# Kernel optimization log

Measured on AMD Instinct MI355X. Metric: run time of the kernel, lower is better.

## Reference

```python
import jax, jax.numpy as jnp
import numpy as np

B = 4096          # batch of vectors
D = 768           # embedding_size
P = 96            # partition (number of sub-quantizers)
C = 256           # centroids per partition
SD = D // P       # sub-vector dim = 8


def setup_inputs() -> dict:
    key = jax.random.key(0)
    k1, k2 = jax.random.split(key)
    vecs = jax.random.normal(k1, (B, D), dtype=jnp.float32)
    # nn.Parameter(torch.empty(P, C, SD).uniform_(-0.1, 0.1))
    codebook = jax.random.uniform(k2, (P, C, SD), dtype=jnp.float32,
                                  minval=-0.1, maxval=0.1)
    return {"vecs": vecs, "codebook": codebook}


def _quantize(vecs, codebook):
    # vecs: [B, D] -> [B, P, SD]
    v = vecs.reshape(vecs.shape[0], P, SD)
    # proba = -sum((v - c)^2) expanded to avoid the [B,P,C,SD] intermediate:
    # ||v||^2 - 2 v.c + ||c||^2  per (b, p, c)
    v_sq = jnp.sum(v * v, axis=-1, keepdims=True)            # [B, P, 1]
    c_sq = jnp.sum(codebook * codebook, axis=-1)             # [P, C]
    vc = jnp.einsum('bpd,pcd->bpc', v, codebook)             # [B, P, C]
    proba = -(v_sq - 2.0 * vc + c_sq[None])                  # [B, P, C]
    assign = jax.nn.softmax(proba, axis=-1)                  # [B, P, C]
    # straight-through estimator: hard one-hot fwd, soft grad
    index = jnp.argmax(assign, axis=-1)                      # [B, P]
    assign_hard = jax.nn.one_hot(index, C, dtype=assign.dtype)
    assign_ste = jax.lax.stop_gradient(assign_hard - assign) + assign
    # reconstruction: [B,P,C] @ [P,C,SD] -> [B,P,SD] -> [B,D]
    q = jnp.einsum('bpc,pcd->bpd', assign_ste, codebook)
    return q.reshape(vecs.shape[0], -1)


def reference(vecs, codebook):
    return _quantize(vecs, codebook)
```

## Files before the change

kernel.cpp:

```cpp
#include <hip/hip_runtime.h>
#include <cmath>

constexpr int B  = 4096;
constexpr int D  = 768;
constexpr int P  = 96;
constexpr int C  = 256;
constexpr int SD = 8;

constexpr int TPB  = 64;
constexpr int ROWS = 4;

__device__ __forceinline__ float tree8(float q0, float q1, float q2, float q3,
                                       float q4, float q5, float q6, float q7)
{
#pragma clang fp contract(off)
    return ((q0 + q1) + (q2 + q3)) + ((q4 + q5) + (q6 + q7));
}

__device__ __forceinline__ float proba_np(const float* __restrict__ cbf,
                                          const float* __restrict__ csq,
                                          int c, float4 va, float4 vb, float vsq)
{
#pragma clang fp contract(off)
    float4 ca = ((const float4*)cbf)[2 * c];
    float4 cb = ((const float4*)cbf)[2 * c + 1];
    float p0 = va.x * ca.x, p1 = va.y * ca.y, p2 = va.z * ca.z, p3 = va.w * ca.w;
    float p4 = vb.x * cb.x, p5 = vb.y * cb.y, p6 = vb.z * cb.z, p7 = vb.w * cb.w;
    float l0 = p0 + p4, l1 = p1 + p5, l2 = p2 + p6, l3 = p3 + p7;
    float vc = (l0 + l2) + (l1 + l3);
    float tt = vsq - 2.0f * vc;
    float u  = tt + csq[c];
    return -u;
}

__device__ __attribute__((noinline))
int exact_search(const float* __restrict__ cbf, const float* __restrict__ csq,
                 float4 va, float4 vb, float vsq)
{
#pragma clang fp contract(off)
    float best = -3.402823466e38f, second = -3.402823466e38f;
    int bi = 0;
    for (int c = 0; c < C; ++c) {
        float pr = proba_np(cbf, csq, c, va, vb, vsq);
        if (pr > best)        { second = best; best = pr; bi = c; }
        else if (pr > second) { second = pr; }
    }
    int idx = bi;

    if (best - second <= 1.0e-6f) {
        float m = best;
        float r0[8] = {0,0,0,0,0,0,0,0};
        float r1[8] = {0,0,0,0,0,0,0,0};
        for (int cg = 0; cg < 16; ++cg) {
            #pragma unroll
            for (int j = 0; j < 8; ++j) {
                float pr = proba_np(cbf, csq, cg * 8 + j, va, vb, vsq);
                r0[j] += expf(pr - m);
            }
        }
        for (int cg = 16; cg < 32; ++cg) {
            #pragma unroll
            for (int j = 0; j < 8; ++j) {
                float pr = proba_np(cbf, csq, cg * 8 + j, va, vb, vsq);
                r1[j] += expf(pr - m);
            }
        }
        float sum = tree8(r0[0],r0[1],r0[2],r0[3],r0[4],r0[5],r0[6],r0[7])
                  + tree8(r1[0],r1[1],r1[2],r1[3],r1[4],r1[5],r1[6],r1[7]);
        float abest = -1.0f;
        int   ai    = 0;
        for (int c = 0; c < C; ++c) {
            float pr = proba_np(cbf, csq, c, va, vb, vsq);
            float e  = expf(pr - m);
            float a  = e / sum;
            if (a > abest) { abest = a; ai = c; }
        }
        idx = ai;
    }
    return idx;
}

__global__ __launch_bounds__(TPB, 8)
void pq_fast_kernel(const float* __restrict__ vecs,
                    const float* __restrict__ codebook,
                    float* __restrict__ out)
{
    __shared__ float cbf [C * SD];
    __shared__ float csqn[C];
    __shared__ float csqh[C];

    const int p = blockIdx.x;
    const int t = threadIdx.x;
    const int base = blockIdx.y * (TPB * ROWS);

    const float4* src = (const float4*)(codebook + (size_t)p * C * SD);
    #pragma unroll
    for (int i = 0; i < 8; ++i)
        ((float4*)cbf)[t + 64 * i] = src[t + 64 * i];
    __syncthreads();

    #pragma unroll
    for (int k = 0; k < 4; ++k) {
        int c = t + 64 * k;
        const float* cc = cbf + c * SD;
        float q0 = cc[0]*cc[0], q1 = cc[1]*cc[1], q2 = cc[2]*cc[2], q3 = cc[3]*cc[3];
        float q4 = cc[4]*cc[4], q5 = cc[5]*cc[5], q6 = cc[6]*cc[6], q7 = cc[7]*cc[7];
        float s = tree8(q0,q1,q2,q3,q4,q5,q6,q7);
        csqn[c] = s;
        csqh[c] = -0.5f * s;
    }
    __syncthreads();

    float4 va[ROWS], vb[ROWS];
    #pragma unroll
    for (int r = 0; r < ROWS; ++r) {
        const float* vptr = vecs + (size_t)(base + 64 * r + t) * D + (size_t)p * SD;
        va[r] = ((const float4*)vptr)[0];
        vb[r] = ((const float4*)vptr)[1];
    }

    float vsq[ROWS];
    #pragma unroll
    for (int r = 0; r < ROWS; ++r) {
        float q0 = va[r].x*va[r].x, q1 = va[r].y*va[r].y,
              q2 = va[r].z*va[r].z, q3 = va[r].w*va[r].w;
        float q4 = vb[r].x*vb[r].x, q5 = vb[r].y*vb[r].y,
              q6 = vb[r].z*vb[r].z, q7 = vb[r].w*vb[r].w;
        vsq[r] = tree8(q0,q1,q2,q3,q4,q5,q6,q7);
    }

    float best[ROWS], second[ROWS];
    int   bi[ROWS];
    #pragma unroll
    for (int r = 0; r < ROWS; ++r) {
        best[r] = -3.402823466e38f; second[r] = -3.402823466e38f; bi[r] = 0;
    }

    #pragma unroll 2
    for (int c = 0; c < C; ++c) {
        float4 ca = ((const float4*)cbf)[2 * c];
        float4 cb = ((const float4*)cbf)[2 * c + 1];
        float  ch = csqh[c];
        #pragma unroll
        for (int r = 0; r < ROWS; ++r) {
            float s = fmaf(va[r].x, ca.x, ch);
            s = fmaf(va[r].y, ca.y, s);
            s = fmaf(va[r].z, ca.z, s);
            s = fmaf(va[r].w, ca.w, s);
            s = fmaf(vb[r].x, cb.x, s);
            s = fmaf(vb[r].y, cb.y, s);
            s = fmaf(vb[r].z, cb.z, s);
            s = fmaf(vb[r].w, cb.w, s);
            bool gt = s > best[r];
            second[r] = fmaxf(second[r], fminf(s, best[r]));
            bi[r]     = gt ? c : bi[r];
            best[r]   = fmaxf(s, best[r]);
        }
    }

    #pragma unroll
    for (int r = 0; r < ROWS; ++r) {
        int idx = bi[r];
        if (best[r] - second[r] <= 2.0e-5f)
            idx = exact_search(cbf, csqn, va[r], vb[r], vsq[r]);
        float4 o0 = ((const float4*)cbf)[2 * idx];
        float4 o1 = ((const float4*)cbf)[2 * idx + 1];
        float4* op = (float4*)(out + (size_t)(base + 64 * r + t) * D + (size_t)p * SD);
        op[0] = o0;
        op[1] = o1;
    }
}

extern "C" void kernel_launch(void* const* d_in, const int* in_sizes, int n_in,
                              void* d_out, int out_size, void* d_ws, size_t ws_size,
                              hipStream_t stream)
{
    const float* vecs     = (const float*)d_in[0];
    const float* codebook = (const float*)d_in[1];
    float*       out      = (float*)d_out;

    dim3 grid(P, B / (TPB * ROWS));
    dim3 block(TPB);
    pq_fast_kernel<<<grid, block, 0, stream>>>(vecs, codebook, out);
}
```

Measured before the change: 193.9 us.

## Split centroid search across four waves with shared-memory argmax merge

Each block now runs four waves. Every wave scans a quarter of the 256 centroids for the same 256 rows, then the partial best/second/index values are merged through shared memory and the final winner is written out. The codebook shared-memory load is amortized over four times as many scanning threads per block, and each thread's serial loop is shortened, giving more parallel work. In exchange it adds an extra barrier, shared-memory traffic for the partials, and a lower occupancy bound. Rows that need the exact fallback now reload their vector from global memory.

```diff
diff --git a/kernel.cpp b/kernel.cpp
--- a/kernel.cpp
+++ b/kernel.cpp
@@ -7,7 +7,9 @@
 constexpr int C  = 256;
 constexpr int SD = 8;
 
-constexpr int TPB  = 64;
+constexpr int TPB  = 256;
+constexpr int WPB  = 4;
+constexpr int CPW  = C / WPB;
 constexpr int ROWS = 4;
 
 __device__ __forceinline__ float tree8(float q0, float q1, float q2, float q3,
@@ -80,53 +82,44 @@
     return idx;
 }
 
-__global__ __launch_bounds__(TPB, 8)
-void pq_fast_kernel(const float* __restrict__ vecs,
-                    const float* __restrict__ codebook,
-                    float* __restrict__ out)
-{
-    __shared__ float cbf [C * SD];
-    __shared__ float csqn[C];
-    __shared__ float csqh[C];
+__global__ __launch_bounds__(TPB, 6)
+void pq_split_kernel(const float* __restrict__ vecs,
+                     const float* __restrict__ codebook,
+                     float* __restrict__ out)
+{
+    __shared__ float  cbf [C * SD];
+    __shared__ float  csqn[C];
+    __shared__ float  csqh[C];
+    __shared__ float2 part_bs[WPB][ROWS][64];
+    __shared__ int    part_i [WPB][ROWS][64];
 
     const int p = blockIdx.x;
     const int t = threadIdx.x;
-    const int base = blockIdx.y * (TPB * ROWS);
+    const int w = t >> 6;
+    const int l = t & 63;
+    const int rowbase = blockIdx.y * (64 * ROWS);
 
     const float4* src = (const float4*)(codebook + (size_t)p * C * SD);
-    #pragma unroll
-    for (int i = 0; i < 8; ++i)
-        ((float4*)cbf)[t + 64 * i] = src[t + 64 * i];
+    ((float4*)cbf)[t]       = src[t];
+    ((float4*)cbf)[t + 256] = src[t + 256];
     __syncthreads();
 
-    #pragma unroll
-    for (int k = 0; k < 4; ++k) {
-        int c = t + 64 * k;
-        const float* cc = cbf + c * SD;
+    {
+        const float* cc = cbf + t * SD;
         float q0 = cc[0]*cc[0], q1 = cc[1]*cc[1], q2 = cc[2]*cc[2], q3 = cc[3]*cc[3];
         float q4 = cc[4]*cc[4], q5 = cc[5]*cc[5], q6 = cc[6]*cc[6], q7 = cc[7]*cc[7];
         float s = tree8(q0,q1,q2,q3,q4,q5,q6,q7);
-        csqn[c] = s;
-        csqh[c] = -0.5f * s;
+        csqn[t] = s;
+        csqh[t] = -0.5f * s;
     }
     __syncthreads();
 
     float4 va[ROWS], vb[ROWS];
     #pragma unroll
     for (int r = 0; r < ROWS; ++r) {
-        const float* vptr = vecs + (size_t)(base + 64 * r + t) * D + (size_t)p * SD;
+        const float* vptr = vecs + (size_t)(rowbase + 64 * r + l) * D + (size_t)p * SD;
         va[r] = ((const float4*)vptr)[0];
         vb[r] = ((const float4*)vptr)[1];
-    }
-
-    float vsq[ROWS];
-    #pragma unroll
-    for (int r = 0; r < ROWS; ++r) {
-        float q0 = va[r].x*va[r].x, q1 = va[r].y*va[r].y,
-              q2 = va[r].z*va[r].z, q3 = va[r].w*va[r].w;
-        float q4 = vb[r].x*vb[r].x, q5 = vb[r].y*vb[r].y,
-              q6 = vb[r].z*vb[r].z, q7 = vb[r].w*vb[r].w;
-        vsq[r] = tree8(q0,q1,q2,q3,q4,q5,q6,q7);
     }
 
     float best[ROWS], second[ROWS];
@@ -136,8 +129,10 @@
         best[r] = -3.402823466e38f; second[r] = -3.402823466e38f; bi[r] = 0;
     }
 
+    const int c0 = w * CPW;
     #pragma unroll 2
-    for (int c = 0; c < C; ++c) {
+    for (int ci = 0; ci < CPW; ++ci) {
+        const int c = c0 + ci;
         float4 ca = ((const float4*)cbf)[2 * c];
         float4 cb = ((const float4*)cbf)[2 * c + 1];
         float  ch = csqh[c];
@@ -160,12 +155,40 @@
 
     #pragma unroll
     for (int r = 0; r < ROWS; ++r) {
-        int idx = bi[r];
-        if (best[r] - second[r] <= 2.0e-5f)
-            idx = exact_search(cbf, csqn, va[r], vb[r], vsq[r]);
+        part_bs[w][r][l] = make_float2(best[r], second[r]);
+        part_i [w][r][l] = bi[r];
+    }
+    __syncthreads();
+
+    {
+        float Bst = -3.402823466e38f, Snd = -3.402823466e38f;
+        int   I   = 0;
+        #pragma unroll
+        for (int ww = 0; ww < WPB; ++ww) {
+            float2 bs = part_bs[ww][w][l];
+            int    iw = part_i [ww][w][l];
+            bool gt = bs.x > Bst;
+            Snd = fmaxf(Snd, fminf(bs.x, Bst));
+            Snd = fmaxf(Snd, bs.y);
+            I   = gt ? iw : I;
+            Bst = fmaxf(Bst, bs.x);
+        }
+
+        const int row = rowbase + t;
+        int idx = I;
+        if (Bst - Snd <= 2.0e-5f) {
+            const float* vptr = vecs + (size_t)row * D + (size_t)p * SD;
+            float4 xa = ((const float4*)vptr)[0];
+            float4 xb = ((const float4*)vptr)[1];
+            float q0 = xa.x*xa.x, q1 = xa.y*xa.y, q2 = xa.z*xa.z, q3 = xa.w*xa.w;
+            float q4 = xb.x*xb.x, q5 = xb.y*xb.y, q6 = xb.z*xb.z, q7 = xb.w*xb.w;
+            float vsq = tree8(q0,q1,q2,q3,q4,q5,q6,q7);
+            idx = exact_search(cbf, csqn, xa, xb, vsq);
+        }
+
         float4 o0 = ((const float4*)cbf)[2 * idx];
         float4 o1 = ((const float4*)cbf)[2 * idx + 1];
-        float4* op = (float4*)(out + (size_t)(base + 64 * r + t) * D + (size_t)p * SD);
+        float4* op = (float4*)(out + (size_t)row * D + (size_t)p * SD);
         op[0] = o0;
         op[1] = o1;
     }
@@ -179,7 +202,7 @@
     const float* codebook = (const float*)d_in[1];
     float*       out      = (float*)d_out;
 
-    dim3 grid(P, B / (TPB * ROWS));
+    dim3 grid(P, B / (64 * ROWS));
     dim3 block(TPB);
-    pq_fast_kernel<<<grid, block, 0, stream>>>(vecs, codebook, out);
-}
+    pq_split_kernel<<<grid, block, 0, stream>>>(vecs, codebook, out);
+}
```

New measurement: 173.0 us. 1.12x faster.

## Stage vector tiles through LDS for coalesced loads and stores across three partitions

Applied to the files above, without the earlier changes.

Each block now covers three partitions (one per wavefront) and 256 rows. It loads a contiguous 96-byte slice of each row into padded shared memory with coalesced float4 accesses, then writes the output back through the same staging buffer. Before, each thread issued strided 32-byte accesses per row. The inner loop also batches four centroid loads before computing. The cost is more shared memory per block, an extra barrier, and lower occupancy (launch bounds 4).

```diff
diff --git a/kernel.cpp b/kernel.cpp
--- a/kernel.cpp
+++ b/kernel.cpp
@@ -7,8 +7,11 @@
 constexpr int C  = 256;
 constexpr int SD = 8;
 
-constexpr int TPB  = 64;
-constexpr int ROWS = 4;
+constexpr int TPB   = 192;
+constexpr int PT    = 3;
+constexpr int RT    = 256;
+constexpr int ROWS  = 4;
+constexpr int VROW  = 28;
 
 __device__ __forceinline__ float tree8(float q0, float q1, float q2, float q3,
                                        float q4, float q5, float q6, float q7)
@@ -80,54 +83,64 @@
     return idx;
 }
 
-__global__ __launch_bounds__(TPB, 8)
-void pq_fast_kernel(const float* __restrict__ vecs,
+__global__ __launch_bounds__(TPB, 4)
+void pq_coal_kernel(const float* __restrict__ vecs,
                     const float* __restrict__ codebook,
                     float* __restrict__ out)
 {
-    __shared__ float cbf [C * SD];
-    __shared__ float csqn[C];
-    __shared__ float csqh[C];
-
-    const int p = blockIdx.x;
-    const int t = threadIdx.x;
-    const int base = blockIdx.y * (TPB * ROWS);
-
-    const float4* src = (const float4*)(codebook + (size_t)p * C * SD);
-    #pragma unroll
-    for (int i = 0; i < 8; ++i)
-        ((float4*)cbf)[t + 64 * i] = src[t + 64 * i];
+    __shared__ float vt  [RT * VROW];
+    __shared__ float cbl [PT * C * SD];
+    __shared__ float csqn[PT * C];
+    __shared__ float csqh[PT * C];
+
+    const int t  = threadIdx.x;
+    const int w  = t >> 6;
+    const int l  = t & 63;
+    const int bx = blockIdx.x;
+    const int rowbase = blockIdx.y * RT;
+    const int t6  = t / 6;
+    const int tm6 = t - 6 * t6;
+
+    {
+        const float4* src = (const float4*)(codebook + (size_t)(3 * bx) * C * SD);
+        float4* dst = (float4*)cbl;
+        #pragma unroll
+        for (int k = 0; k < 8; ++k)
+            dst[t + TPB * k] = src[t + TPB * k];
+    }
+    {
+        const float4* src = (const float4*)vecs;
+        #pragma unroll
+        for (int k = 0; k < 8; ++k) {
+            int row = k * 32 + t6;
+            float4 x = src[(size_t)(rowbase + row) * (D / 4) + bx * 6 + tm6];
+            *(float4*)(vt + row * VROW + tm6 * 4) = x;
+        }
+    }
     __syncthreads();
 
     #pragma unroll
     for (int k = 0; k < 4; ++k) {
-        int c = t + 64 * k;
-        const float* cc = cbf + c * SD;
+        int c = t + TPB * k;
+        const float* cc = cbl + c * SD;
         float q0 = cc[0]*cc[0], q1 = cc[1]*cc[1], q2 = cc[2]*cc[2], q3 = cc[3]*cc[3];
         float q4 = cc[4]*cc[4], q5 = cc[5]*cc[5], q6 = cc[6]*cc[6], q7 = cc[7]*cc[7];
         float s = tree8(q0,q1,q2,q3,q4,q5,q6,q7);
         csqn[c] = s;
         csqh[c] = -0.5f * s;
     }
+
+    float4 va[ROWS], vb[ROWS];
+    #pragma unroll
+    for (int r = 0; r < ROWS; ++r) {
+        const float* vp = vt + (64 * r + l) * VROW + w * SD;
+        va[r] = *(const float4*)(vp);
+        vb[r] = *(const float4*)(vp + 4);
+    }
     __syncthreads();
 
-    float4 va[ROWS], vb[ROWS];
-    #pragma unroll
-    for (int r = 0; r < ROWS; ++r) {
-        const float* vptr = vecs + (size_t)(base + 64 * r + t) * D + (size_t)p * SD;
-        va[r] = ((const float4*)vptr)[0];
-        vb[r] = ((const float4*)vptr)[1];
-    }
-
-    float vsq[ROWS];
-    #pragma unroll
-    for (int r = 0; r < ROWS; ++r) {
-        float q0 = va[r].x*va[r].x, q1 = va[r].y*va[r].y,
-              q2 = va[r].z*va[r].z, q3 = va[r].w*va[r].w;
-        float q4 = vb[r].x*vb[r].x, q5 = vb[r].y*vb[r].y,
-              q6 = vb[r].z*vb[r].z, q7 = vb[r].w*vb[r].w;
-        vsq[r] = tree8(q0,q1,q2,q3,q4,q5,q6,q7);
-    }
+    const float4* CB = (const float4*)(cbl + w * C * SD);
+    const float*  CH = csqh + w * C;
 
     float best[ROWS], second[ROWS];
     int   bi[ROWS];
@@ -136,38 +149,64 @@
         best[r] = -3.402823466e38f; second[r] = -3.402823466e38f; bi[r] = 0;
     }
 
-    #pragma unroll 2
-    for (int c = 0; c < C; ++c) {
-        float4 ca = ((const float4*)cbf)[2 * c];
-        float4 cb = ((const float4*)cbf)[2 * c + 1];
-        float  ch = csqh[c];
-        #pragma unroll
-        for (int r = 0; r < ROWS; ++r) {
-            float s = fmaf(va[r].x, ca.x, ch);
-            s = fmaf(va[r].y, ca.y, s);
-            s = fmaf(va[r].z, ca.z, s);
-            s = fmaf(va[r].w, ca.w, s);
-            s = fmaf(vb[r].x, cb.x, s);
-            s = fmaf(vb[r].y, cb.y, s);
-            s = fmaf(vb[r].z, cb.z, s);
-            s = fmaf(vb[r].w, cb.w, s);
-            bool gt = s > best[r];
-            second[r] = fmaxf(second[r], fminf(s, best[r]));
-            bi[r]     = gt ? c : bi[r];
-            best[r]   = fmaxf(s, best[r]);
-        }
-    }
-
+    for (int c = 0; c < C; c += 4) {
+        float4 A[4], Bv[4];
+        float  H[4];
+        #pragma unroll
+        for (int u = 0; u < 4; ++u) {
+            A[u]  = CB[2 * (c + u)];
+            Bv[u] = CB[2 * (c + u) + 1];
+            H[u]  = CH[c + u];
+        }
+        #pragma unroll
+        for (int u = 0; u < 4; ++u) {
+            #pragma unroll
+            for (int r = 0; r < ROWS; ++r) {
+                float s = fmaf(va[r].x, A[u].x, H[u]);
+                s = fmaf(va[r].y, A[u].y, s);
+                s = fmaf(va[r].z, A[u].z, s);
+                s = fmaf(va[r].w, A[u].w, s);
+                s = fmaf(vb[r].x, Bv[u].x, s);
+                s = fmaf(vb[r].y, Bv[u].y, s);
+                s = fmaf(vb[r].z, Bv[u].z, s);
+                s = fmaf(vb[r].w, Bv[u].w, s);
+                bool gt = s > best[r];
+                second[r] = fmaxf(second[r], fminf(s, best[r]));
+                bi[r]     = gt ? (c + u) : bi[r];
+                best[r]   = fmaxf(s, best[r]);
+            }
+        }
+    }
+
+    const float* cbf_w = cbl + w * C * SD;
+    const float* csq_w = csqn + w * C;
     #pragma unroll
     for (int r = 0; r < ROWS; ++r) {
         int idx = bi[r];
-        if (best[r] - second[r] <= 2.0e-5f)
-            idx = exact_search(cbf, csqn, va[r], vb[r], vsq[r]);
-        float4 o0 = ((const float4*)cbf)[2 * idx];
-        float4 o1 = ((const float4*)cbf)[2 * idx + 1];
-        float4* op = (float4*)(out + (size_t)(base + 64 * r + t) * D + (size_t)p * SD);
-        op[0] = o0;
-        op[1] = o1;
+        if (best[r] - second[r] <= 2.0e-5f) {
+            float q0 = va[r].x*va[r].x, q1 = va[r].y*va[r].y,
+                  q2 = va[r].z*va[r].z, q3 = va[r].w*va[r].w;
+            float q4 = vb[r].x*vb[r].x, q5 = vb[r].y*vb[r].y,
+                  q6 = vb[r].z*vb[r].z, q7 = vb[r].w*vb[r].w;
+            float vsq = tree8(q0,q1,q2,q3,q4,q5,q6,q7);
+            idx = exact_search(cbf_w, csq_w, va[r], vb[r], vsq);
+        }
+        float4 o0 = ((const float4*)cbf_w)[2 * idx];
+        float4 o1 = ((const float4*)cbf_w)[2 * idx + 1];
+        float* op = vt + (64 * r + l) * VROW + w * SD;
+        *(float4*)(op)     = o0;
+        *(float4*)(op + 4) = o1;
+    }
+    __syncthreads();
+
+    {
+        float4* dst = (float4*)out;
+        #pragma unroll
+        for (int k = 0; k < 8; ++k) {
+            int row = k * 32 + t6;
+            float4 x = *(const float4*)(vt + row * VROW + tm6 * 4);
+            dst[(size_t)(rowbase + row) * (D / 4) + bx * 6 + tm6] = x;
+        }
     }
 }
 
@@ -179,7 +218,7 @@
     const float* codebook = (const float*)d_in[1];
     float*       out      = (float*)d_out;
 
-    dim3 grid(P, B / (TPB * ROWS));
+    dim3 grid(P / PT, B / RT);
     dim3 block(TPB);
-    pq_fast_kernel<<<grid, block, 0, stream>>>(vecs, codebook, out);
-}
+    pq_coal_kernel<<<grid, block, 0, stream>>>(vecs, codebook, out);
+}
```

New measurement: 191.7 us. Within noise of the previous version (-1.2%).

## Stream codebook from global in register double-buffer, enlarge blocks to 128 threads

Applied to the files above, without the earlier changes.

The main distance loop now reads codebook entries straight from global memory with uniform addresses, software-prefetching the next group of four centroids into registers while computing the current group, instead of reading them from LDS. Blocks grow to 128 threads with launch bounds lowered to 3, the vector loads are issued before the shared-memory fill, and the vector norm is computed only on the rare tie path. The aim is to cut LDS read traffic and hide load latency. In exchange it uses more registers, lowers occupancy, and relies on the cache to serve the repeated codebook reads.

```diff
diff --git a/kernel.cpp b/kernel.cpp
--- a/kernel.cpp
+++ b/kernel.cpp
@@ -7,7 +7,7 @@
 constexpr int C  = 256;
 constexpr int SD = 8;
 
-constexpr int TPB  = 64;
+constexpr int TPB  = 128;
 constexpr int ROWS = 4;
 
 __device__ __forceinline__ float tree8(float q0, float q1, float q2, float q3,
@@ -80,8 +80,8 @@
     return idx;
 }
 
-__global__ __launch_bounds__(TPB, 8)
-void pq_fast_kernel(const float* __restrict__ vecs,
+__global__ __launch_bounds__(TPB, 3)
+void pq_smem_kernel(const float* __restrict__ vecs,
                     const float* __restrict__ codebook,
                     float* __restrict__ out)
 {
@@ -91,17 +91,25 @@
 
     const int p = blockIdx.x;
     const int t = threadIdx.x;
-    const int base = blockIdx.y * (TPB * ROWS);
+    const int rowbase = blockIdx.y * (TPB * ROWS);
 
-    const float4* src = (const float4*)(codebook + (size_t)p * C * SD);
+    float4 va[ROWS], vb[ROWS];
     #pragma unroll
-    for (int i = 0; i < 8; ++i)
-        ((float4*)cbf)[t + 64 * i] = src[t + 64 * i];
+    for (int r = 0; r < ROWS; ++r) {
+        const float* vptr = vecs + (size_t)(rowbase + TPB * r + t) * D + (size_t)p * SD;
+        va[r] = ((const float4*)vptr)[0];
+        vb[r] = ((const float4*)vptr)[1];
+    }
+
+    const float4* CBg = (const float4*)(codebook + (size_t)p * C * SD);
+    #pragma unroll
+    for (int k = 0; k < 4; ++k)
+        ((float4*)cbf)[t + TPB * k] = CBg[t + TPB * k];
     __syncthreads();
 
     #pragma unroll
-    for (int k = 0; k < 4; ++k) {
-        int c = t + 64 * k;
+    for (int k = 0; k < 2; ++k) {
+        int c = t + TPB * k;
         const float* cc = cbf + c * SD;
         float q0 = cc[0]*cc[0], q1 = cc[1]*cc[1], q2 = cc[2]*cc[2], q3 = cc[3]*cc[3];
         float q4 = cc[4]*cc[4], q5 = cc[5]*cc[5], q6 = cc[6]*cc[6], q7 = cc[7]*cc[7];
@@ -111,24 +119,6 @@
     }
     __syncthreads();
 
-    float4 va[ROWS], vb[ROWS];
-    #pragma unroll
-    for (int r = 0; r < ROWS; ++r) {
-        const float* vptr = vecs + (size_t)(base + 64 * r + t) * D + (size_t)p * SD;
-        va[r] = ((const float4*)vptr)[0];
-        vb[r] = ((const float4*)vptr)[1];
-    }
-
-    float vsq[ROWS];
-    #pragma unroll
-    for (int r = 0; r < ROWS; ++r) {
-        float q0 = va[r].x*va[r].x, q1 = va[r].y*va[r].y,
-              q2 = va[r].z*va[r].z, q3 = va[r].w*va[r].w;
-        float q4 = vb[r].x*vb[r].x, q5 = vb[r].y*vb[r].y,
-              q6 = vb[r].z*vb[r].z, q7 = vb[r].w*vb[r].w;
-        vsq[r] = tree8(q0,q1,q2,q3,q4,q5,q6,q7);
-    }
-
     float best[ROWS], second[ROWS];
     int   bi[ROWS];
     #pragma unroll
@@ -136,36 +126,56 @@
         best[r] = -3.402823466e38f; second[r] = -3.402823466e38f; bi[r] = 0;
     }
 
-    #pragma unroll 2
-    for (int c = 0; c < C; ++c) {
-        float4 ca = ((const float4*)cbf)[2 * c];
-        float4 cb = ((const float4*)cbf)[2 * c + 1];
-        float  ch = csqh[c];
+    float4 A[8], N[8];
+    #pragma unroll
+    for (int i = 0; i < 8; ++i) A[i] = CBg[i];
+
+    for (int g = 0; g < 64; ++g) {
+        const int gn = (g + 1) & 63;
         #pragma unroll
-        for (int r = 0; r < ROWS; ++r) {
-            float s = fmaf(va[r].x, ca.x, ch);
-            s = fmaf(va[r].y, ca.y, s);
-            s = fmaf(va[r].z, ca.z, s);
-            s = fmaf(va[r].w, ca.w, s);
-            s = fmaf(vb[r].x, cb.x, s);
-            s = fmaf(vb[r].y, cb.y, s);
-            s = fmaf(vb[r].z, cb.z, s);
-            s = fmaf(vb[r].w, cb.w, s);
-            bool gt = s > best[r];
-            second[r] = fmaxf(second[r], fminf(s, best[r]));
-            bi[r]     = gt ? c : bi[r];
-            best[r]   = fmaxf(s, best[r]);
+        for (int i = 0; i < 8; ++i) N[i] = CBg[8 * gn + i];
+
+        float4 H4 = ((const float4*)csqh)[g];
+        float  H[4] = { H4.x, H4.y, H4.z, H4.w };
+
+        #pragma unroll
+        for (int u = 0; u < 4; ++u) {
+            const float4 ca = A[2 * u];
+            const float4 cb = A[2 * u + 1];
+            #pragma unroll
+            for (int r = 0; r < ROWS; ++r) {
+                float s = fmaf(va[r].x, ca.x, H[u]);
+                s = fmaf(va[r].y, ca.y, s);
+                s = fmaf(va[r].z, ca.z, s);
+                s = fmaf(va[r].w, ca.w, s);
+                s = fmaf(vb[r].x, cb.x, s);
+                s = fmaf(vb[r].y, cb.y, s);
+                s = fmaf(vb[r].z, cb.z, s);
+                s = fmaf(vb[r].w, cb.w, s);
+                bool gt = s > best[r];
+                second[r] = fmaxf(second[r], fminf(s, best[r]));
+                bi[r]     = gt ? (4 * g + u) : bi[r];
+                best[r]   = fmaxf(s, best[r]);
+            }
         }
+        #pragma unroll
+        for (int i = 0; i < 8; ++i) A[i] = N[i];
     }
 
     #pragma unroll
     for (int r = 0; r < ROWS; ++r) {
         int idx = bi[r];
-        if (best[r] - second[r] <= 2.0e-5f)
-            idx = exact_search(cbf, csqn, va[r], vb[r], vsq[r]);
+        if (best[r] - second[r] <= 2.0e-5f) {
+            float q0 = va[r].x*va[r].x, q1 = va[r].y*va[r].y,
+                  q2 = va[r].z*va[r].z, q3 = va[r].w*va[r].w;
+            float q4 = vb[r].x*vb[r].x, q5 = vb[r].y*vb[r].y,
+                  q6 = vb[r].z*vb[r].z, q7 = vb[r].w*vb[r].w;
+            float vsq = tree8(q0,q1,q2,q3,q4,q5,q6,q7);
+            idx = exact_search(cbf, csqn, va[r], vb[r], vsq);
+        }
         float4 o0 = ((const float4*)cbf)[2 * idx];
         float4 o1 = ((const float4*)cbf)[2 * idx + 1];
-        float4* op = (float4*)(out + (size_t)(base + 64 * r + t) * D + (size_t)p * SD);
+        float4* op = (float4*)(out + (size_t)(rowbase + TPB * r + t) * D + (size_t)p * SD);
         op[0] = o0;
         op[1] = o1;
     }
@@ -181,5 +191,5 @@
 
     dim3 grid(P, B / (TPB * ROWS));
     dim3 block(TPB);
-    pq_fast_kernel<<<grid, block, 0, stream>>>(vecs, codebook, out);
+    pq_smem_kernel<<<grid, block, 0, stream>>>(vecs, codebook, out);
 }
```

Result: faster. 187.0 us (-3.6%).
